# Kernel tuning notes

Hardware: AMD Instinct MI355X
Metric: run time of the kernel (lower is better)

The kernel has to match this reference:

```python
import jax, jax.numpy as jnp
import numpy as np

C = 1.0          # Poincare ball curvature
H = 8            # num_heads
EPS = 1e-15
DELTA = 1e-7
SC = np.sqrt(C)  # sqrt curvature


def _norm(x):
    return jnp.sqrt(jnp.clip(jnp.sum(x * x, -1, keepdims=True), 1e-15))


def mobius_add(x, y):
    xy = jnp.sum(x * y, -1, keepdims=True)
    x2 = jnp.sum(x * x, -1, keepdims=True)
    y2 = jnp.sum(y * y, -1, keepdims=True)
    num = (1 + 2 * C * xy + C * y2) * x + (1 - C * x2) * y
    den = 1 + 2 * C * xy + C * C * x2 * y2
    return num / (den + EPS)


def mobius_matvec(W, x):
    xn = _norm(x)
    mx = x @ W.T
    mxn = _norm(mx)
    arg = jnp.clip(SC * xn, None, 1 - 1e-5)
    return jnp.tanh(mxn / xn * jnp.arctanh(arg)) * mx / (mxn * SC)


def logmap0(x):
    xn = _norm(x)
    return jnp.arctanh(jnp.clip(SC * xn, None, 1 - 1e-5)) * x / (SC * xn)


def expmap0(u):
    un = _norm(u)
    return jnp.tanh(SC * un) * u / (SC * un)


def hyp_linear(W, b, x):
    return mobius_add(mobius_matvec(W, x), b)


def setup_inputs() -> dict:
    key = jax.random.key(0)
    ks = jax.random.split(key, 5)
    B, S, E = 2, 512, 256
    x = jax.random.normal(ks[0], (B, S, E), jnp.float32) * 0.02  # inside unit ball
    scale = float(np.sqrt(6.0 / (E + E)))  # xavier uniform bound
    Wq = jax.random.uniform(ks[1], (E, E), jnp.float32, -scale, scale)
    Wk = jax.random.uniform(ks[2], (E, E), jnp.float32, -scale, scale)
    Wv = jax.random.uniform(ks[3], (E, E), jnp.float32, -scale, scale)
    Wo = jax.random.uniform(ks[4], (E, E), jnp.float32, -scale, scale)
    z = jnp.zeros((E,), jnp.float32)
    head_scaling = jnp.ones((H, 1, 1), jnp.float32)
    return {"x": x, "Wq": Wq, "bq": z, "Wk": Wk, "bk": z, "Wv": Wv, "bv": z,
            "Wo": Wo, "bo": z, "head_scaling": head_scaling}


def reference(x, Wq, bq, Wk, bk, Wv, bv, Wo, bo, head_scaling):
    B, S, E = x.shape
    D = E // H
    q = hyp_linear(Wq, bq, x).reshape(B, S, H, D).transpose(0, 2, 1, 3)  # (B,H,S,D)
    k = hyp_linear(Wk, bk, x).reshape(B, S, H, D).transpose(0, 2, 1, 3)
    v = hyp_linear(Wv, bv, x).reshape(B, S, H, D).transpose(0, 2, 1, 3)
    max_norm = (1 - 1e-5) / SC
    q = jnp.minimum(q, max_norm)  # elementwise clamp_max, faithful to source
    k = jnp.minimum(k, max_norm)
    qn = C * jnp.sum(q * q, -1)[..., :, None]   # (B,H,Sq,1)
    kn = C * jnp.sum(k * k, -1)[..., None, :]   # (B,H,1,Sk)
    # pairwise mobius_add(-k, q): (B,H,Sq,Sk,D)
    diff = mobius_add(-k[:, :, None, :, :], q[:, :, :, None, :])
    dn = C * jnp.sum(diff * diff, -1)           # (B,H,Sq,Sk)
    denom = (1 - qn) * (1 - kn) + EPS
    a = jnp.maximum(1 + 2 * dn / denom, 1 + DELTA)
    dist = jnp.log(a + jnp.sqrt(a * a - 1))     # acosh
    scores = -dist / (head_scaling * np.sqrt(D))
    w = jax.nn.softmax(scores, -1)
    out = expmap0(jnp.einsum('bhqk,bhkd->bhqd', w, logmap0(v)))
    out = out.transpose(0, 2, 1, 3).reshape(B, S, E)
    return hyp_linear(Wo, bo, out)
```

## Files before the change

kernel.cpp:

```cpp
#include <hip/hip_runtime.h>
#include <math.h>

#define Ec 256
#define Sc 512
#define Bc 2
#define Hc 8
#define Dc 32
#define MAXNORM (1.0f - 1e-5f)
#define NEc (Bc * Sc * Ec)
#define KSQ 2
#define KSO 4
#define NROWS (Bc * Hc * Sc)

__device__ __forceinline__ float fullWaveSum(float v) {
#pragma unroll
  for (int m = 32; m >= 1; m >>= 1) v += __shfl_xor(v, m, 64);
  return v;
}
__device__ __forceinline__ float halfWaveSum(float v) {
#pragma unroll
  for (int m = 16; m >= 1; m >>= 1) v += __shfl_xor(v, m, 64);
  return v;
}
__device__ __forceinline__ float atanh_fast(float z) {
  return 0.5f * __logf((1.0f + z) / (1.0f - z));
}
__device__ __forceinline__ float tanh_fast(float a) {
  float e = __expf(-2.0f * a);
  return (1.0f - e) / (1.0f + e);
}

__global__ __launch_bounds__(128) void gemm_xwt(
    const float* __restrict__ X,
    const float* __restrict__ W0, const float* __restrict__ W1,
    const float* __restrict__ W2,
    float* __restrict__ O0, float* __restrict__ O1, float* __restrict__ O2,
    const int nk) {
  const int tid = threadIdx.x;
  const int bx = blockIdx.x;
  const int by = blockIdx.y;
  const int kz = blockIdx.z;
  const int mat = by >> 2;
  const int cb0 = (by & 3) * 64;
  const int rb0 = bx * 32;
  const int kk0 = kz * 64 * nk;
  const float* __restrict__ W = (mat == 0) ? W0 : (mat == 1) ? W1 : W2;
  float* __restrict__ O = ((mat == 0) ? O0 : (mat == 1) ? O1 : O2) + (size_t)kz * NEc;

  __shared__ float Xs[64][36];
  __shared__ float Ws[64][68];

  const int f4 = tid & 15;
  const int sub = tid >> 4;
  const int ty = tid >> 4;
  const int tx = tid & 15;

  float acc[4][4];
#pragma unroll
  for (int i = 0; i < 4; ++i)
#pragma unroll
    for (int j = 0; j < 4; ++j) acc[i][j] = 0.f;

  for (int c = 0; c < nk; ++c) {
    const int kk = kk0 + c * 64;
    __syncthreads();
#pragma unroll
    for (int i = 0; i < 4; ++i) {
      int row = sub + i * 8;
      float4 v = *(const float4*)&X[(size_t)(rb0 + row) * Ec + kk + f4 * 4];
      Xs[f4 * 4 + 0][row] = v.x;
      Xs[f4 * 4 + 1][row] = v.y;
      Xs[f4 * 4 + 2][row] = v.z;
      Xs[f4 * 4 + 3][row] = v.w;
    }
#pragma unroll
    for (int i = 0; i < 8; ++i) {
      int col = sub + i * 8;
      float4 v = *(const float4*)&W[(size_t)(cb0 + col) * Ec + kk + f4 * 4];
      Ws[f4 * 4 + 0][col] = v.x;
      Ws[f4 * 4 + 1][col] = v.y;
      Ws[f4 * 4 + 2][col] = v.z;
      Ws[f4 * 4 + 3][col] = v.w;
    }
    __syncthreads();
#pragma unroll 8
    for (int k = 0; k < 64; ++k) {
      float4 a = *(const float4*)&Xs[k][ty * 4];
      float4 b = *(const float4*)&Ws[k][tx * 4];
      float av[4] = {a.x, a.y, a.z, a.w};
      float bv[4] = {b.x, b.y, b.z, b.w};
#pragma unroll
      for (int i = 0; i < 4; ++i)
#pragma unroll
        for (int j = 0; j < 4; ++j) acc[i][j] = fmaf(av[i], bv[j], acc[i][j]);
    }
  }
#pragma unroll
  for (int i = 0; i < 4; ++i) {
    float4 o = make_float4(acc[i][0], acc[i][1], acc[i][2], acc[i][3]);
    *(float4*)&O[(size_t)(rb0 + ty * 4 + i) * Ec + cb0 + tx * 4] = o;
  }
}

__global__ __launch_bounds__(256) void qkv_stats(
    const float* __restrict__ x,
    const float* __restrict__ mxq, const float* __restrict__ mxk,
    const float* __restrict__ mxv,
    const float* __restrict__ bq, const float* __restrict__ bk,
    const float* __restrict__ bv,
    float* __restrict__ qo, float* __restrict__ ko, float* __restrict__ lvo,
    float* __restrict__ qno, float* __restrict__ kno) {
  const int t = threadIdx.x;
  const int row = blockIdx.x;
  const int b = row >> 9;
  const int s = row & (Sc - 1);
  const size_t idx = (size_t)row * Ec + t;
  const float xv = x[idx];
  float mq = 0.f, mk = 0.f, mv = 0.f;
#pragma unroll
  for (int p = 0; p < KSQ; ++p) {
    mq += mxq[idx + (size_t)p * NEc];
    mk += mxk[idx + (size_t)p * NEc];
    mv += mxv[idx + (size_t)p * NEc];
  }
  const float bb[3] = {bq[t], bk[t], bv[t]};
  const float mvals[3] = {mq, mk, mv};

  float vals[10] = {xv * xv,
                    mq * mq, mq * bb[0], bb[0] * bb[0],
                    mk * mk, mk * bb[1], bb[1] * bb[1],
                    mv * mv, mv * bb[2], bb[2] * bb[2]};
  __shared__ float red[10][4];
  __shared__ float fin[10];
#pragma unroll
  for (int i = 0; i < 10; ++i) {
    float v = fullWaveSum(vals[i]);
    if ((t & 63) == 0) red[i][t >> 6] = v;
  }
  __syncthreads();
  if (t < 10) fin[t] = red[t][0] + red[t][1] + red[t][2] + red[t][3];
  __syncthreads();

  const float x2 = fin[0];
  const float xn = sqrtf(fmaxf(x2, 1e-15f));
  const float at = atanh_fast(fminf(xn, MAXNORM));
  const int h = t >> 5;

#pragma unroll
  for (int m = 0; m < 3; ++m) {
    float mx2 = fin[1 + 3 * m];
    float mxb = fin[2 + 3 * m];
    float b2 = fin[3 + 3 * m];
    float mxn = sqrtf(fmaxf(mx2, 1e-15f));
    float scl = tanh_fast((mxn / xn) * at) / mxn;
    float mvv = scl * mvals[m];
    float X2 = scl * scl * mx2;
    float XY = scl * mxb;
    float numc = 1.0f + 2.0f * XY + b2;
    float den = 1.0f + 2.0f * XY + X2 * b2 + 1e-15f;
    float res = (numc * mvv + (1.0f - X2) * bb[m]) / den;
    if (m < 2) {
      res = fminf(res, MAXNORM);
      float s2 = halfWaveSum(res * res);
      if (m == 0) {
        qo[idx] = res;
        if ((t & 31) == 0) qno[(b * Hc + h) * Sc + s] = s2;
      } else {
        ko[idx] = res;
        if ((t & 31) == 0) kno[(b * Hc + h) * Sc + s] = s2;
      }
    } else {
      float vn2 = halfWaveSum(res * res);
      float vn = sqrtf(fmaxf(vn2, 1e-15f));
      float f = atanh_fast(fminf(vn, MAXNORM)) / vn;
      lvo[idx] = f * res;
    }
  }
}

__global__ __launch_bounds__(256) void score_kernel(
    const float* __restrict__ q, const float* __restrict__ k,
    const float* __restrict__ qn, const float* __restrict__ kn,
    const float* __restrict__ hs, float* __restrict__ P) {
  const int tid = threadIdx.x;
  const int sk0 = blockIdx.x * 64;
  const int sq0 = blockIdx.y * 64;
  const int bh = blockIdx.z;
  const int b = bh >> 3;
  const int h = bh & 7;

  __shared__ float Qs[64][32];
  __shared__ float Ks[64][32];

#pragma unroll
  for (int i = 0; i < 2; ++i) {
    int qi = tid + i * 256;
    int r = qi >> 3;
    int fd = qi & 7;
    int fsw = fd ^ ((r >> 2) & 7);
    float4 v = *(const float4*)&q[(size_t)(b * Sc + sq0 + r) * Ec + h * Dc + fd * 4];
    *(float4*)&Qs[r][fsw * 4] = v;
    float4 w = *(const float4*)&k[(size_t)(b * Sc + sk0 + r) * Ec + h * Dc + fd * 4];
    *(float4*)&Ks[r][fsw * 4] = w;
  }
  __syncthreads();

  const int ty = tid >> 4;
  const int tx = tid & 15;

  float acc[4][4];
#pragma unroll
  for (int i = 0; i < 4; ++i)
#pragma unroll
    for (int j = 0; j < 4; ++j) acc[i][j] = 0.f;

#pragma unroll
  for (int fd = 0; fd < 8; ++fd) {
    const int qsw = (fd ^ (ty & 7)) * 4;
    const int ksw = (fd ^ (tx & 7)) * 4;
    float4 a[4], bb[4];
#pragma unroll
    for (int i = 0; i < 4; ++i) a[i] = *(const float4*)&Qs[ty * 4 + i][qsw];
#pragma unroll
    for (int j = 0; j < 4; ++j) bb[j] = *(const float4*)&Ks[tx * 4 + j][ksw];
#pragma unroll
    for (int i = 0; i < 4; ++i)
#pragma unroll
      for (int j = 0; j < 4; ++j) {
        acc[i][j] = fmaf(a[i].x, bb[j].x, acc[i][j]);
        acc[i][j] = fmaf(a[i].y, bb[j].y, acc[i][j]);
        acc[i][j] = fmaf(a[i].z, bb[j].z, acc[i][j]);
        acc[i][j] = fmaf(a[i].w, bb[j].w, acc[i][j]);
      }
  }

  const float sinv = -1.0f / (hs[h] * sqrtf((float)Dc));
  float qnv[4], knv[4];
#pragma unroll
  for (int i = 0; i < 4; ++i) qnv[i] = qn[bh * Sc + sq0 + ty * 4 + i];
#pragma unroll
  for (int j = 0; j < 4; ++j) knv[j] = kn[bh * Sc + sk0 + tx * 4 + j];

#pragma unroll
  for (int i = 0; i < 4; ++i) {
    const float q2 = qnv[i];
    const float omq = 1.0f - q2;
    float4 o;
    float po[4];
#pragma unroll
    for (int j = 0; j < 4; ++j) {
      const float k2 = knv[j];
      const float kq = acc[i][j];
      const float omk = 1.0f - k2;
      float s2x2 = fmaf(-4.0f, kq, 2.0f * k2 + 2.0f * q2);
      float dden = fmaf(k2, q2, fmaf(-2.0f, kq, 1.0f)) + 1e-15f;
      float Pd = fmaf(dden, omk * omq, 1e-20f);
      float rp = __builtin_amdgcn_rcpf(Pd);
      float tt = fmaxf(s2x2 * rp, 1e-7f);
      float z = (1.0f + tt) + sqrtf(fmaf(tt, tt, tt + tt));
      po[j] = __builtin_amdgcn_exp2f(sinv * __builtin_amdgcn_logf(z));
    }
    o.x = po[0]; o.y = po[1]; o.z = po[2]; o.w = po[3];
    *(float4*)&P[((size_t)bh * Sc + sq0 + ty * 4 + i) * Sc + sk0 + tx * 4] = o;
  }
}

__global__ __launch_bounds__(256) void pv_kernel(
    const float* __restrict__ P, const float* __restrict__ lv,
    float* __restrict__ out) {
  const int tid = threadIdx.x;
  const int sq0 = blockIdx.x * 16;
  const int bh = blockIdx.y;
  const int b = bh >> 3;
  const int h = bh & 7;
  const int js = tid >> 5;
  const int rg = (tid >> 3) & 3;
  const int dq = tid & 7;

  __shared__ float Ps[16][68];
  __shared__ float lvs[64][36];
  __shared__ float accm[16][8][32];
  __shared__ float lsb[16][9];

  float4 acc[4];
#pragma unroll
  for (int i = 0; i < 4; ++i) acc[i] = make_float4(0.f, 0.f, 0.f, 0.f);
  float lsum4[4] = {0.f, 0.f, 0.f, 0.f};

#pragma unroll 1
  for (int t = 0; t < 8; ++t) {
    const int j0g = t * 64;
    {
      int pr = tid >> 4, pc = tid & 15;
      *(float4*)&Ps[pr][pc * 4] =
          *(const float4*)&P[((size_t)bh * Sc + sq0 + pr) * Sc + j0g + pc * 4];
#pragma unroll
      for (int i = 0; i < 2; ++i) {
        int qi = tid + i * 256;
        int lr = qi >> 3, lc = qi & 7;
        *(float4*)&lvs[lr][lc * 4] =
            *(const float4*)&lv[(size_t)(b * Sc + j0g + lr) * Ec + h * Dc + lc * 4];
      }
    }
    __syncthreads();

#pragma unroll
    for (int j4 = 0; j4 < 2; ++j4) {
      const int j0 = js * 8 + j4 * 4;
      float4 p[4], l[4];
#pragma unroll
      for (int i = 0; i < 4; ++i) p[i] = *(const float4*)&Ps[rg * 4 + i][j0];
#pragma unroll
      for (int c = 0; c < 4; ++c) l[c] = *(const float4*)&lvs[j0 + c][dq * 4];
#pragma unroll
      for (int i = 0; i < 4; ++i) {
        lsum4[i] += (p[i].x + p[i].y) + (p[i].z + p[i].w);
        acc[i].x = fmaf(p[i].x, l[0].x, acc[i].x);
        acc[i].y = fmaf(p[i].x, l[0].y, acc[i].y);
        acc[i].z = fmaf(p[i].x, l[0].z, acc[i].z);
        acc[i].w = fmaf(p[i].x, l[0].w, acc[i].w);
        acc[i].x = fmaf(p[i].y, l[1].x, acc[i].x);
        acc[i].y = fmaf(p[i].y, l[1].y, acc[i].y);
        acc[i].z = fmaf(p[i].y, l[1].z, acc[i].z);
        acc[i].w = fmaf(p[i].y, l[1].w, acc[i].w);
        acc[i].x = fmaf(p[i].z, l[2].x, acc[i].x);
        acc[i].y = fmaf(p[i].z, l[2].y, acc[i].y);
        acc[i].z = fmaf(p[i].z, l[2].z, acc[i].z);
        acc[i].w = fmaf(p[i].z, l[2].w, acc[i].w);
        acc[i].x = fmaf(p[i].w, l[3].x, acc[i].x);
        acc[i].y = fmaf(p[i].w, l[3].y, acc[i].y);
        acc[i].z = fmaf(p[i].w, l[3].z, acc[i].z);
        acc[i].w = fmaf(p[i].w, l[3].w, acc[i].w);
      }
    }
    __syncthreads();
  }

#pragma unroll
  for (int i = 0; i < 4; ++i)
    *(float4*)&accm[rg * 4 + i][js][dq * 4] = acc[i];
  if (dq == 0) {
#pragma unroll
    for (int i = 0; i < 4; ++i) lsb[rg * 4 + i][js] = lsum4[i];
  }
  __syncthreads();

  const int r2 = tid >> 4;
  const int dd = tid & 15;
  float o0 = 0.f, o1 = 0.f, ls = 0.f;
#pragma unroll
  for (int g = 0; g < 8; ++g) {
    float2 a2 = *(const float2*)&accm[r2][g][dd * 2];
    o0 += a2.x;
    o1 += a2.y;
    ls += lsb[r2][g];
  }
  const float li = 1.0f / ls;
  o0 *= li;
  o1 *= li;
  float un2 = fmaf(o0, o0, o1 * o1);
#pragma unroll
  for (int m = 8; m >= 1; m >>= 1) un2 += __shfl_xor(un2, m, 16);
  float un = sqrtf(fmaxf(un2, 1e-15f));
  float f = tanh_fast(un) / un;
  float2 ov = make_float2(o0 * f, o1 * f);
  *(float2*)&out[(size_t)(b * Sc + sq0 + r2) * Ec + h * Dc + dd * 2] = ov;
}

__global__ __launch_bounds__(256) void proj_stats(
    const float* __restrict__ xin, const float* __restrict__ mx,
    const float* __restrict__ bo, float* __restrict__ out) {
  const int t = threadIdx.x;
  const int row = blockIdx.x;
  const size_t idx = (size_t)row * Ec + t;
  const float xv = xin[idx];
  float m = 0.f;
#pragma unroll
  for (int p = 0; p < KSO; ++p) m += mx[idx + (size_t)p * NEc];
  const float bb = bo[t];
  float vals[4] = {xv * xv, m * m, m * bb, bb * bb};
  __shared__ float red[4][4];
  __shared__ float fin[4];
#pragma unroll
  for (int i = 0; i < 4; ++i) {
    float v = fullWaveSum(vals[i]);
    if ((t & 63) == 0) red[i][t >> 6] = v;
  }
  __syncthreads();
  if (t < 4) fin[t] = red[t][0] + red[t][1] + red[t][2] + red[t][3];
  __syncthreads();

  float x2 = fin[0], mx2 = fin[1], mxb = fin[2], b2 = fin[3];
  float xn = sqrtf(fmaxf(x2, 1e-15f));
  float mxn = sqrtf(fmaxf(mx2, 1e-15f));
  float scl = tanh_fast((mxn / xn) * atanh_fast(fminf(xn, MAXNORM))) / mxn;
  float mvv = scl * m;
  float X2 = scl * scl * mx2;
  float XY = scl * mxb;
  float numc = 1.0f + 2.0f * XY + b2;
  float den = 1.0f + 2.0f * XY + X2 * b2 + 1e-15f;
  out[idx] = (numc * mvv + (1.0f - X2) * bb) / den;
}

extern "C" void kernel_launch(void* const* d_in, const int* in_sizes, int n_in,
                              void* d_out, int out_size, void* d_ws, size_t ws_size,
                              hipStream_t stream) {
  (void)in_sizes; (void)n_in; (void)out_size; (void)ws_size;
  const float* x  = (const float*)d_in[0];
  const float* Wq = (const float*)d_in[1];
  const float* bq = (const float*)d_in[2];
  const float* Wk = (const float*)d_in[3];
  const float* bk = (const float*)d_in[4];
  const float* Wv = (const float*)d_in[5];
  const float* bv = (const float*)d_in[6];
  const float* Wo = (const float*)d_in[7];
  const float* bo = (const float*)d_in[8];
  const float* hs = (const float*)d_in[9];

  float* ws = (float*)d_ws;
  const int NE = NEc;
  const int NH = NROWS;
  float* mxq = ws;
  float* mxk = mxq + KSQ * NE;
  float* mxv = mxk + KSQ * NE;
  float* mxo = mxv + KSQ * NE;
  float* qb  = mxo + KSO * NE;
  float* kb  = qb + NE;
  float* lvb = kb + NE;
  float* aob = lvb + NE;
  float* qnb = aob + NE;
  float* knb = qnb + NH;
  float* Pb  = knb + NH;

  const int M = Bc * Sc;

  gemm_xwt<<<dim3(M / 32, 12, KSQ), 128, 0, stream>>>(x, Wq, Wk, Wv,
                                                      mxq, mxk, mxv, 2);
  qkv_stats<<<M, 256, 0, stream>>>(x, mxq, mxk, mxv, bq, bk, bv,
                                   qb, kb, lvb, qnb, knb);
  score_kernel<<<dim3(8, 8, 16), 256, 0, stream>>>(qb, kb, qnb, knb, hs, Pb);
  pv_kernel<<<dim3(32, 16), 256, 0, stream>>>(Pb, lvb, aob);
  gemm_xwt<<<dim3(M / 32, 4, KSO), 128, 0, stream>>>(aob, Wo, Wo, Wo,
                                                     mxo, mxo, mxo, 1);
  proj_stats<<<M, 256, 0, stream>>>(aob, mxo, bo, (float*)d_out);
}
```

Measured before the change: 124.7 us.

## Fuse hyperbolic score and PV kernels into single flash-style attention kernel

```diff
diff --git a/kernel.cpp b/kernel.cpp
--- a/kernel.cpp
+++ b/kernel.cpp
@@ -178,79 +178,80 @@
   }
 }
 
-__global__ __launch_bounds__(256) void score_kernel(
+__global__ __launch_bounds__(256) void attn_fused(
     const float* __restrict__ q, const float* __restrict__ k,
-    const float* __restrict__ qn, const float* __restrict__ kn,
-    const float* __restrict__ hs, float* __restrict__ P) {
+    const float* __restrict__ lv, const float* __restrict__ qn,
+    const float* __restrict__ kn, const float* __restrict__ hs,
+    float* __restrict__ out) {
   const int tid = threadIdx.x;
-  const int sk0 = blockIdx.x * 64;
-  const int sq0 = blockIdx.y * 64;
-  const int bh = blockIdx.z;
+  const int sq0 = blockIdx.x * 16;
+  const int bh = blockIdx.y;
   const int b = bh >> 3;
   const int h = bh & 7;
 
-  __shared__ float Qs[64][32];
-  __shared__ float Ks[64][32];
-
-#pragma unroll
-  for (int i = 0; i < 2; ++i) {
-    int qi = tid + i * 256;
-    int r = qi >> 3;
-    int fd = qi & 7;
-    int fsw = fd ^ ((r >> 2) & 7);
-    float4 v = *(const float4*)&q[(size_t)(b * Sc + sq0 + r) * Ec + h * Dc + fd * 4];
-    *(float4*)&Qs[r][fsw * 4] = v;
-    float4 w = *(const float4*)&k[(size_t)(b * Sc + sk0 + r) * Ec + h * Dc + fd * 4];
-    *(float4*)&Ks[r][fsw * 4] = w;
-  }
-  __syncthreads();
-
-  const int ty = tid >> 4;
-  const int tx = tid & 15;
-
-  float acc[4][4];
-#pragma unroll
-  for (int i = 0; i < 4; ++i)
-#pragma unroll
-    for (int j = 0; j < 4; ++j) acc[i][j] = 0.f;
-
-#pragma unroll
-  for (int fd = 0; fd < 8; ++fd) {
-    const int qsw = (fd ^ (ty & 7)) * 4;
-    const int ksw = (fd ^ (tx & 7)) * 4;
-    float4 a[4], bb[4];
-#pragma unroll
-    for (int i = 0; i < 4; ++i) a[i] = *(const float4*)&Qs[ty * 4 + i][qsw];
-#pragma unroll
-    for (int j = 0; j < 4; ++j) bb[j] = *(const float4*)&Ks[tx * 4 + j][ksw];
-#pragma unroll
-    for (int i = 0; i < 4; ++i)
-#pragma unroll
-      for (int j = 0; j < 4; ++j) {
-        acc[i][j] = fmaf(a[i].x, bb[j].x, acc[i][j]);
-        acc[i][j] = fmaf(a[i].y, bb[j].y, acc[i][j]);
-        acc[i][j] = fmaf(a[i].z, bb[j].z, acc[i][j]);
-        acc[i][j] = fmaf(a[i].w, bb[j].w, acc[i][j]);
-      }
-  }
-
+  __shared__ float Qst[Dc][17];
+  __shared__ float Kst[Dc][68];
+  __shared__ float LVs[2][64][36];
+  __shared__ float Pst[64][17];
+  __shared__ float knS[64];
+  __shared__ float redD[4][16];
+  __shared__ float redN[4][16];
+
+  const int r = tid & 15;
+  const int c4 = tid >> 4;
+
+  if (tid < 128) {
+    int qr = tid >> 3, dq = tid & 7;
+    float4 v = *(const float4*)&q[(size_t)(b * Sc + sq0 + qr) * Ec + h * Dc + dq * 4];
+    Qst[dq * 4 + 0][qr] = v.x;
+    Qst[dq * 4 + 1][qr] = v.y;
+    Qst[dq * 4 + 2][qr] = v.z;
+    Qst[dq * 4 + 3][qr] = v.w;
+  }
+  const float q2 = qn[bh * Sc + sq0 + r];
+  const float omq = 1.0f - q2;
   const float sinv = -1.0f / (hs[h] * sqrtf((float)Dc));
-  float qnv[4], knv[4];
-#pragma unroll
-  for (int i = 0; i < 4; ++i) qnv[i] = qn[bh * Sc + sq0 + ty * 4 + i];
-#pragma unroll
-  for (int j = 0; j < 4; ++j) knv[j] = kn[bh * Sc + sk0 + tx * 4 + j];
-
-#pragma unroll
-  for (int i = 0; i < 4; ++i) {
-    const float q2 = qnv[i];
-    const float omq = 1.0f - q2;
-    float4 o;
-    float po[4];
+
+  float out0 = 0.f, out1 = 0.f, den_acc = 0.f;
+
+  const int srow = tid >> 3;
+  const int sdq = tid & 7;
+
+  for (int t = 0; t < 8; ++t) {
+    const int j0 = t * 64;
+    const int buf = t & 1;
+#pragma unroll
+    for (int i = 0; i < 2; ++i) {
+      int row = srow + i * 32;
+      const size_t gidx = (size_t)(b * Sc + j0 + row) * Ec + h * Dc + sdq * 4;
+      float4 kv = *(const float4*)&k[gidx];
+      Kst[sdq * 4 + 0][row] = kv.x;
+      Kst[sdq * 4 + 1][row] = kv.y;
+      Kst[sdq * 4 + 2][row] = kv.z;
+      Kst[sdq * 4 + 3][row] = kv.w;
+      float4 lvv = *(const float4*)&lv[gidx];
+      *(float4*)&LVs[buf][row][sdq * 4] = lvv;
+    }
+    if (tid < 64) knS[tid] = kn[bh * Sc + j0 + tid];
+    __syncthreads();
+
+    float p[4] = {0.f, 0.f, 0.f, 0.f};
+#pragma unroll
+    for (int kk = 0; kk < Dc; ++kk) {
+      float qv = Qst[kk][r];
+      float4 kvv = *(const float4*)&Kst[kk][c4 * 4];
+      p[0] = fmaf(qv, kvv.x, p[0]);
+      p[1] = fmaf(qv, kvv.y, p[1]);
+      p[2] = fmaf(qv, kvv.z, p[2]);
+      p[3] = fmaf(qv, kvv.w, p[3]);
+    }
+    float4 k2v = *(const float4*)&knS[c4 * 4];
+    float kk2[4] = {k2v.x, k2v.y, k2v.z, k2v.w};
+    float ps = 0.f;
 #pragma unroll
     for (int j = 0; j < 4; ++j) {
-      const float k2 = knv[j];
-      const float kq = acc[i][j];
+      const float k2 = kk2[j];
+      const float kq = p[j];
       const float omk = 1.0f - k2;
       float s2x2 = fmaf(-4.0f, kq, 2.0f * k2 + 2.0f * q2);
       float dden = fmaf(k2, q2, fmaf(-2.0f, kq, 1.0f)) + 1e-15f;
@@ -258,113 +259,42 @@
       float rp = __builtin_amdgcn_rcpf(Pd);
       float tt = fmaxf(s2x2 * rp, 1e-7f);
       float z = (1.0f + tt) + sqrtf(fmaf(tt, tt, tt + tt));
-      po[j] = __builtin_amdgcn_exp2f(sinv * __builtin_amdgcn_logf(z));
-    }
-    o.x = po[0]; o.y = po[1]; o.z = po[2]; o.w = po[3];
-    *(float4*)&P[((size_t)bh * Sc + sq0 + ty * 4 + i) * Sc + sk0 + tx * 4] = o;
-  }
-}
-
-__global__ __launch_bounds__(256) void pv_kernel(
-    const float* __restrict__ P, const float* __restrict__ lv,
-    float* __restrict__ out) {
-  const int tid = threadIdx.x;
-  const int sq0 = blockIdx.x * 16;
-  const int bh = blockIdx.y;
-  const int b = bh >> 3;
-  const int h = bh & 7;
-  const int js = tid >> 5;
-  const int rg = (tid >> 3) & 3;
-  const int dq = tid & 7;
-
-  __shared__ float Ps[16][68];
-  __shared__ float lvs[64][36];
-  __shared__ float accm[16][8][32];
-  __shared__ float lsb[16][9];
-
-  float4 acc[4];
-#pragma unroll
-  for (int i = 0; i < 4; ++i) acc[i] = make_float4(0.f, 0.f, 0.f, 0.f);
-  float lsum4[4] = {0.f, 0.f, 0.f, 0.f};
-
-#pragma unroll 1
-  for (int t = 0; t < 8; ++t) {
-    const int j0g = t * 64;
-    {
-      int pr = tid >> 4, pc = tid & 15;
-      *(float4*)&Ps[pr][pc * 4] =
-          *(const float4*)&P[((size_t)bh * Sc + sq0 + pr) * Sc + j0g + pc * 4];
-#pragma unroll
-      for (int i = 0; i < 2; ++i) {
-        int qi = tid + i * 256;
-        int lr = qi >> 3, lc = qi & 7;
-        *(float4*)&lvs[lr][lc * 4] =
-            *(const float4*)&lv[(size_t)(b * Sc + j0g + lr) * Ec + h * Dc + lc * 4];
-      }
-    }
+      float po = __builtin_amdgcn_exp2f(sinv * __builtin_amdgcn_logf(z));
+      Pst[c4 * 4 + j][r] = po;
+      ps += po;
+    }
+    den_acc += ps;
     __syncthreads();
 
-#pragma unroll
-    for (int j4 = 0; j4 < 2; ++j4) {
-      const int j0 = js * 8 + j4 * 4;
-      float4 p[4], l[4];
-#pragma unroll
-      for (int i = 0; i < 4; ++i) p[i] = *(const float4*)&Ps[rg * 4 + i][j0];
-#pragma unroll
-      for (int c = 0; c < 4; ++c) l[c] = *(const float4*)&lvs[j0 + c][dq * 4];
-#pragma unroll
-      for (int i = 0; i < 4; ++i) {
-        lsum4[i] += (p[i].x + p[i].y) + (p[i].z + p[i].w);
-        acc[i].x = fmaf(p[i].x, l[0].x, acc[i].x);
-        acc[i].y = fmaf(p[i].x, l[0].y, acc[i].y);
-        acc[i].z = fmaf(p[i].x, l[0].z, acc[i].z);
-        acc[i].w = fmaf(p[i].x, l[0].w, acc[i].w);
-        acc[i].x = fmaf(p[i].y, l[1].x, acc[i].x);
-        acc[i].y = fmaf(p[i].y, l[1].y, acc[i].y);
-        acc[i].z = fmaf(p[i].y, l[1].z, acc[i].z);
-        acc[i].w = fmaf(p[i].y, l[1].w, acc[i].w);
-        acc[i].x = fmaf(p[i].z, l[2].x, acc[i].x);
-        acc[i].y = fmaf(p[i].z, l[2].y, acc[i].y);
-        acc[i].z = fmaf(p[i].z, l[2].z, acc[i].z);
-        acc[i].w = fmaf(p[i].z, l[2].w, acc[i].w);
-        acc[i].x = fmaf(p[i].w, l[3].x, acc[i].x);
-        acc[i].y = fmaf(p[i].w, l[3].y, acc[i].y);
-        acc[i].z = fmaf(p[i].w, l[3].z, acc[i].z);
-        acc[i].w = fmaf(p[i].w, l[3].w, acc[i].w);
-      }
-    }
-    __syncthreads();
-  }
-
-#pragma unroll
-  for (int i = 0; i < 4; ++i)
-    *(float4*)&accm[rg * 4 + i][js][dq * 4] = acc[i];
-  if (dq == 0) {
-#pragma unroll
-    for (int i = 0; i < 4; ++i) lsb[rg * 4 + i][js] = lsum4[i];
-  }
-  __syncthreads();
-
-  const int r2 = tid >> 4;
-  const int dd = tid & 15;
-  float o0 = 0.f, o1 = 0.f, ls = 0.f;
-#pragma unroll
-  for (int g = 0; g < 8; ++g) {
-    float2 a2 = *(const float2*)&accm[r2][g][dd * 2];
-    o0 += a2.x;
-    o1 += a2.y;
-    ls += lsb[r2][g];
-  }
-  const float li = 1.0f / ls;
-  o0 *= li;
-  o1 *= li;
+#pragma unroll 8
+    for (int j = 0; j < 64; ++j) {
+      float pj = Pst[j][r];
+      float2 l2 = *(const float2*)&LVs[buf][j][c4 * 2];
+      out0 = fmaf(pj, l2.x, out0);
+      out1 = fmaf(pj, l2.y, out1);
+    }
+  }
+
+  float d = den_acc;
+  d += __shfl_xor(d, 16, 64);
+  d += __shfl_xor(d, 32, 64);
+  const int wv = tid >> 6;
+  if ((tid & 63) < 16) redD[wv][r] = d;
+  __syncthreads();
+  const float den = redD[0][r] + redD[1][r] + redD[2][r] + redD[3][r];
+  const float li = 1.0f / den;
+  float o0 = out0 * li, o1 = out1 * li;
+
   float un2 = fmaf(o0, o0, o1 * o1);
-#pragma unroll
-  for (int m = 8; m >= 1; m >>= 1) un2 += __shfl_xor(un2, m, 16);
+  un2 += __shfl_xor(un2, 16, 64);
+  un2 += __shfl_xor(un2, 32, 64);
+  if ((tid & 63) < 16) redN[wv][r] = un2;
+  __syncthreads();
+  un2 = redN[0][r] + redN[1][r] + redN[2][r] + redN[3][r];
   float un = sqrtf(fmaxf(un2, 1e-15f));
   float f = tanh_fast(un) / un;
   float2 ov = make_float2(o0 * f, o1 * f);
-  *(float2*)&out[(size_t)(b * Sc + sq0 + r2) * Ec + h * Dc + dd * 2] = ov;
+  *(float2*)&out[(size_t)(b * Sc + sq0 + r) * Ec + h * Dc + c4 * 2] = ov;
 }
 
 __global__ __launch_bounds__(256) void proj_stats(
@@ -430,7 +360,6 @@
   float* aob = lvb + NE;
   float* qnb = aob + NE;
   float* knb = qnb + NH;
-  float* Pb  = knb + NH;
 
   const int M = Bc * Sc;
 
@@ -438,8 +367,7 @@
                                                       mxq, mxk, mxv, 2);
   qkv_stats<<<M, 256, 0, stream>>>(x, mxq, mxk, mxv, bq, bk, bv,
                                    qb, kb, lvb, qnb, knb);
-  score_kernel<<<dim3(8, 8, 16), 256, 0, stream>>>(qb, kb, qnb, knb, hs, Pb);
-  pv_kernel<<<dim3(32, 16), 256, 0, stream>>>(Pb, lvb, aob);
+  attn_fused<<<dim3(32, 16), 256, 0, stream>>>(qb, kb, lvb, qnb, knb, hs, aob);
   gemm_xwt<<<dim3(M / 32, 4, KSO), 128, 0, stream>>>(aob, Wo, Wo, Wo,
                                                      mxo, mxo, mxo, 1);
   proj_stats<<<M, 256, 0, stream>>>(aob, mxo, bo, (float*)d_out);
```

Result: slower. 133.8 us (+7.2%).

## Fuse score and PV kernels into one attention kernel without materialized P

Applied to the files above, without the earlier changes.

```diff
diff --git a/kernel.cpp b/kernel.cpp
--- a/kernel.cpp
+++ b/kernel.cpp
@@ -11,6 +11,8 @@
 #define KSQ 2
 #define KSO 4
 #define NROWS (Bc * Hc * Sc)
+#define KT 128
+#define NT (Sc / KT)
 
 __device__ __forceinline__ float fullWaveSum(float v) {
 #pragma unroll
@@ -178,140 +180,149 @@
   }
 }
 
-__global__ __launch_bounds__(256) void score_kernel(
+__global__ __launch_bounds__(256, 2) void attn_fused(
     const float* __restrict__ q, const float* __restrict__ k,
-    const float* __restrict__ qn, const float* __restrict__ kn,
-    const float* __restrict__ hs, float* __restrict__ P) {
-  const int tid = threadIdx.x;
-  const int sk0 = blockIdx.x * 64;
-  const int sq0 = blockIdx.y * 64;
-  const int bh = blockIdx.z;
-  const int b = bh >> 3;
-  const int h = bh & 7;
-
-  __shared__ float Qs[64][32];
-  __shared__ float Ks[64][32];
-
-#pragma unroll
-  for (int i = 0; i < 2; ++i) {
-    int qi = tid + i * 256;
-    int r = qi >> 3;
-    int fd = qi & 7;
-    int fsw = fd ^ ((r >> 2) & 7);
-    float4 v = *(const float4*)&q[(size_t)(b * Sc + sq0 + r) * Ec + h * Dc + fd * 4];
-    *(float4*)&Qs[r][fsw * 4] = v;
-    float4 w = *(const float4*)&k[(size_t)(b * Sc + sk0 + r) * Ec + h * Dc + fd * 4];
-    *(float4*)&Ks[r][fsw * 4] = w;
-  }
-  __syncthreads();
-
-  const int ty = tid >> 4;
-  const int tx = tid & 15;
-
-  float acc[4][4];
-#pragma unroll
-  for (int i = 0; i < 4; ++i)
-#pragma unroll
-    for (int j = 0; j < 4; ++j) acc[i][j] = 0.f;
-
-#pragma unroll
-  for (int fd = 0; fd < 8; ++fd) {
-    const int qsw = (fd ^ (ty & 7)) * 4;
-    const int ksw = (fd ^ (tx & 7)) * 4;
-    float4 a[4], bb[4];
-#pragma unroll
-    for (int i = 0; i < 4; ++i) a[i] = *(const float4*)&Qs[ty * 4 + i][qsw];
-#pragma unroll
-    for (int j = 0; j < 4; ++j) bb[j] = *(const float4*)&Ks[tx * 4 + j][ksw];
-#pragma unroll
-    for (int i = 0; i < 4; ++i)
-#pragma unroll
-      for (int j = 0; j < 4; ++j) {
-        acc[i][j] = fmaf(a[i].x, bb[j].x, acc[i][j]);
-        acc[i][j] = fmaf(a[i].y, bb[j].y, acc[i][j]);
-        acc[i][j] = fmaf(a[i].z, bb[j].z, acc[i][j]);
-        acc[i][j] = fmaf(a[i].w, bb[j].w, acc[i][j]);
-      }
-  }
-
-  const float sinv = -1.0f / (hs[h] * sqrtf((float)Dc));
-  float qnv[4], knv[4];
-#pragma unroll
-  for (int i = 0; i < 4; ++i) qnv[i] = qn[bh * Sc + sq0 + ty * 4 + i];
-#pragma unroll
-  for (int j = 0; j < 4; ++j) knv[j] = kn[bh * Sc + sk0 + tx * 4 + j];
-
-#pragma unroll
-  for (int i = 0; i < 4; ++i) {
-    const float q2 = qnv[i];
-    const float omq = 1.0f - q2;
-    float4 o;
-    float po[4];
-#pragma unroll
-    for (int j = 0; j < 4; ++j) {
-      const float k2 = knv[j];
-      const float kq = acc[i][j];
-      const float omk = 1.0f - k2;
-      float s2x2 = fmaf(-4.0f, kq, 2.0f * k2 + 2.0f * q2);
-      float dden = fmaf(k2, q2, fmaf(-2.0f, kq, 1.0f)) + 1e-15f;
-      float Pd = fmaf(dden, omk * omq, 1e-20f);
-      float rp = __builtin_amdgcn_rcpf(Pd);
-      float tt = fmaxf(s2x2 * rp, 1e-7f);
-      float z = (1.0f + tt) + sqrtf(fmaf(tt, tt, tt + tt));
-      po[j] = __builtin_amdgcn_exp2f(sinv * __builtin_amdgcn_logf(z));
-    }
-    o.x = po[0]; o.y = po[1]; o.z = po[2]; o.w = po[3];
-    *(float4*)&P[((size_t)bh * Sc + sq0 + ty * 4 + i) * Sc + sk0 + tx * 4] = o;
-  }
-}
-
-__global__ __launch_bounds__(256) void pv_kernel(
-    const float* __restrict__ P, const float* __restrict__ lv,
+    const float* __restrict__ lv, const float* __restrict__ qn,
+    const float* __restrict__ kn, const float* __restrict__ hs,
     float* __restrict__ out) {
   const int tid = threadIdx.x;
   const int sq0 = blockIdx.x * 16;
   const int bh = blockIdx.y;
   const int b = bh >> 3;
   const int h = bh & 7;
+
+  __shared__ float Qst[16][36];
+  __shared__ float Kst[32][132];
+  __shared__ float LVs[128][36];
+  __shared__ float Pst[16][132];
+  __shared__ float knS[128];
+  __shared__ float accm[16][8][32];
+  __shared__ float lsb[16][9];
+
+  const int r2 = tid >> 5;
+  const int c4 = tid & 31;
   const int js = tid >> 5;
   const int rg = (tid >> 3) & 3;
   const int dq = tid & 7;
-
-  __shared__ float Ps[16][68];
-  __shared__ float lvs[64][36];
-  __shared__ float accm[16][8][32];
-  __shared__ float lsb[16][9];
+  const int rr = tid >> 1;
+  const int half = tid & 1;
+
+  if (tid < 128) {
+    int qr = tid >> 3, dqq = tid & 7;
+    *(float4*)&Qst[qr][dqq * 4] =
+        *(const float4*)&q[(size_t)(b * Sc + sq0 + qr) * Ec + h * Dc + dqq * 4];
+  }
+  __syncthreads();
+  float4 qv0[8], qv1[8];
+#pragma unroll
+  for (int fd = 0; fd < 8; ++fd) {
+    qv0[fd] = *(const float4*)&Qst[2 * r2 + 0][fd * 4];
+    qv1[fd] = *(const float4*)&Qst[2 * r2 + 1][fd * 4];
+  }
+  const float q20 = qn[bh * Sc + sq0 + 2 * r2];
+  const float q21 = qn[bh * Sc + sq0 + 2 * r2 + 1];
+  const float omq0 = 1.0f - q20;
+  const float omq1 = 1.0f - q21;
+  const float sinv = -1.0f / (hs[h] * sqrtf((float)Dc));
 
   float4 acc[4];
 #pragma unroll
   for (int i = 0; i < 4; ++i) acc[i] = make_float4(0.f, 0.f, 0.f, 0.f);
   float lsum4[4] = {0.f, 0.f, 0.f, 0.f};
 
-#pragma unroll 1
-  for (int t = 0; t < 8; ++t) {
-    const int j0g = t * 64;
+  for (int t = 0; t < NT; ++t) {
+    const int j0g = t * KT;
+    __syncthreads();
     {
-      int pr = tid >> 4, pc = tid & 15;
-      *(float4*)&Ps[pr][pc * 4] =
-          *(const float4*)&P[((size_t)bh * Sc + sq0 + pr) * Sc + j0g + pc * 4];
-#pragma unroll
-      for (int i = 0; i < 2; ++i) {
-        int qi = tid + i * 256;
-        int lr = qi >> 3, lc = qi & 7;
-        *(float4*)&lvs[lr][lc * 4] =
-            *(const float4*)&lv[(size_t)(b * Sc + j0g + lr) * Ec + h * Dc + lc * 4];
+      const size_t gbase = (size_t)(b * Sc + j0g + rr) * Ec + h * Dc;
+#pragma unroll
+      for (int i = 0; i < 4; ++i) {
+        const int dqq = half * 4 + i;
+        float4 kv = *(const float4*)&k[gbase + dqq * 4];
+        Kst[dqq * 4 + 0][rr] = kv.x;
+        Kst[dqq * 4 + 1][rr] = kv.y;
+        Kst[dqq * 4 + 2][rr] = kv.z;
+        Kst[dqq * 4 + 3][rr] = kv.w;
+        *(float4*)&LVs[rr][dqq * 4] = *(const float4*)&lv[gbase + dqq * 4];
       }
+      if (tid < 128) knS[tid] = kn[bh * Sc + j0g + tid];
     }
     __syncthreads();
 
-#pragma unroll
-    for (int j4 = 0; j4 < 2; ++j4) {
-      const int j0 = js * 8 + j4 * 4;
+    float p0[4] = {0.f, 0.f, 0.f, 0.f};
+    float p1[4] = {0.f, 0.f, 0.f, 0.f};
+#pragma unroll
+    for (int fd = 0; fd < 8; ++fd) {
+      float4 k0 = *(const float4*)&Kst[fd * 4 + 0][c4 * 4];
+      float4 k1 = *(const float4*)&Kst[fd * 4 + 1][c4 * 4];
+      float4 k2 = *(const float4*)&Kst[fd * 4 + 2][c4 * 4];
+      float4 k3 = *(const float4*)&Kst[fd * 4 + 3][c4 * 4];
+      float4 a0 = qv0[fd];
+      float4 a1 = qv1[fd];
+      p0[0] = fmaf(a0.x, k0.x, p0[0]); p0[0] = fmaf(a0.y, k1.x, p0[0]);
+      p0[0] = fmaf(a0.z, k2.x, p0[0]); p0[0] = fmaf(a0.w, k3.x, p0[0]);
+      p0[1] = fmaf(a0.x, k0.y, p0[1]); p0[1] = fmaf(a0.y, k1.y, p0[1]);
+      p0[1] = fmaf(a0.z, k2.y, p0[1]); p0[1] = fmaf(a0.w, k3.y, p0[1]);
+      p0[2] = fmaf(a0.x, k0.z, p0[2]); p0[2] = fmaf(a0.y, k1.z, p0[2]);
+      p0[2] = fmaf(a0.z, k2.z, p0[2]); p0[2] = fmaf(a0.w, k3.z, p0[2]);
+      p0[3] = fmaf(a0.x, k0.w, p0[3]); p0[3] = fmaf(a0.y, k1.w, p0[3]);
+      p0[3] = fmaf(a0.z, k2.w, p0[3]); p0[3] = fmaf(a0.w, k3.w, p0[3]);
+      p1[0] = fmaf(a1.x, k0.x, p1[0]); p1[0] = fmaf(a1.y, k1.x, p1[0]);
+      p1[0] = fmaf(a1.z, k2.x, p1[0]); p1[0] = fmaf(a1.w, k3.x, p1[0]);
+      p1[1] = fmaf(a1.x, k0.y, p1[1]); p1[1] = fmaf(a1.y, k1.y, p1[1]);
+      p1[1] = fmaf(a1.z, k2.y, p1[1]); p1[1] = fmaf(a1.w, k3.y, p1[1]);
+      p1[2] = fmaf(a1.x, k0.z, p1[2]); p1[2] = fmaf(a1.y, k1.z, p1[2]);
+      p1[2] = fmaf(a1.z, k2.z, p1[2]); p1[2] = fmaf(a1.w, k3.z, p1[2]);
+      p1[3] = fmaf(a1.x, k0.w, p1[3]); p1[3] = fmaf(a1.y, k1.w, p1[3]);
+      p1[3] = fmaf(a1.z, k2.w, p1[3]); p1[3] = fmaf(a1.w, k3.w, p1[3]);
+    }
+
+    float4 k2v = *(const float4*)&knS[c4 * 4];
+    const float kk2[4] = {k2v.x, k2v.y, k2v.z, k2v.w};
+    {
+      float po[4];
+#pragma unroll
+      for (int j = 0; j < 4; ++j) {
+        const float k2 = kk2[j];
+        const float kq = p0[j];
+        const float omk = 1.0f - k2;
+        float s2x2 = fmaf(-4.0f, kq, 2.0f * k2 + 2.0f * q20);
+        float dden = fmaf(k2, q20, fmaf(-2.0f, kq, 1.0f)) + 1e-15f;
+        float Pd = fmaf(dden, omk * omq0, 1e-20f);
+        float rp = __builtin_amdgcn_rcpf(Pd);
+        float tt = fmaxf(s2x2 * rp, 1e-7f);
+        float z = (1.0f + tt) + sqrtf(fmaf(tt, tt, tt + tt));
+        po[j] = __builtin_amdgcn_exp2f(sinv * __builtin_amdgcn_logf(z));
+      }
+      *(float4*)&Pst[2 * r2 + 0][c4 * 4] = make_float4(po[0], po[1], po[2], po[3]);
+    }
+    {
+      float po[4];
+#pragma unroll
+      for (int j = 0; j < 4; ++j) {
+        const float k2 = kk2[j];
+        const float kq = p1[j];
+        const float omk = 1.0f - k2;
+        float s2x2 = fmaf(-4.0f, kq, 2.0f * k2 + 2.0f * q21);
+        float dden = fmaf(k2, q21, fmaf(-2.0f, kq, 1.0f)) + 1e-15f;
+        float Pd = fmaf(dden, omk * omq1, 1e-20f);
+        float rp = __builtin_amdgcn_rcpf(Pd);
+        float tt = fmaxf(s2x2 * rp, 1e-7f);
+        float z = (1.0f + tt) + sqrtf(fmaf(tt, tt, tt + tt));
+        po[j] = __builtin_amdgcn_exp2f(sinv * __builtin_amdgcn_logf(z));
+      }
+      *(float4*)&Pst[2 * r2 + 1][c4 * 4] = make_float4(po[0], po[1], po[2], po[3]);
+    }
+    __syncthreads();
+
+#pragma unroll
+    for (int j4 = 0; j4 < 4; ++j4) {
+      const int jl = js * 16 + j4 * 4;
       float4 p[4], l[4];
 #pragma unroll
-      for (int i = 0; i < 4; ++i) p[i] = *(const float4*)&Ps[rg * 4 + i][j0];
-#pragma unroll
-      for (int c = 0; c < 4; ++c) l[c] = *(const float4*)&lvs[j0 + c][dq * 4];
+      for (int i = 0; i < 4; ++i) p[i] = *(const float4*)&Pst[rg * 4 + i][jl];
+#pragma unroll
+      for (int c = 0; c < 4; ++c) l[c] = *(const float4*)&LVs[jl + c][dq * 4];
 #pragma unroll
       for (int i = 0; i < 4; ++i) {
         lsum4[i] += (p[i].x + p[i].y) + (p[i].z + p[i].w);
@@ -333,7 +344,6 @@
         acc[i].w = fmaf(p[i].w, l[3].w, acc[i].w);
       }
     }
-    __syncthreads();
   }
 
 #pragma unroll
@@ -345,15 +355,15 @@
   }
   __syncthreads();
 
-  const int r2 = tid >> 4;
+  const int r2e = tid >> 4;
   const int dd = tid & 15;
   float o0 = 0.f, o1 = 0.f, ls = 0.f;
 #pragma unroll
   for (int g = 0; g < 8; ++g) {
-    float2 a2 = *(const float2*)&accm[r2][g][dd * 2];
+    float2 a2 = *(const float2*)&accm[r2e][g][dd * 2];
     o0 += a2.x;
     o1 += a2.y;
-    ls += lsb[r2][g];
+    ls += lsb[r2e][g];
   }
   const float li = 1.0f / ls;
   o0 *= li;
@@ -364,7 +374,7 @@
   float un = sqrtf(fmaxf(un2, 1e-15f));
   float f = tanh_fast(un) / un;
   float2 ov = make_float2(o0 * f, o1 * f);
-  *(float2*)&out[(size_t)(b * Sc + sq0 + r2) * Ec + h * Dc + dd * 2] = ov;
+  *(float2*)&out[(size_t)(b * Sc + sq0 + r2e) * Ec + h * Dc + dd * 2] = ov;
 }
 
 __global__ __launch_bounds__(256) void proj_stats(
@@ -430,7 +440,6 @@
   float* aob = lvb + NE;
   float* qnb = aob + NE;
   float* knb = qnb + NH;
-  float* Pb  = knb + NH;
 
   const int M = Bc * Sc;
 
@@ -438,8 +447,7 @@
                                                       mxq, mxk, mxv, 2);
   qkv_stats<<<M, 256, 0, stream>>>(x, mxq, mxk, mxv, bq, bk, bv,
                                    qb, kb, lvb, qnb, knb);
-  score_kernel<<<dim3(8, 8, 16), 256, 0, stream>>>(qb, kb, qnb, knb, hs, Pb);
-  pv_kernel<<<dim3(32, 16), 256, 0, stream>>>(Pb, lvb, aob);
+  attn_fused<<<dim3(32, 16), 256, 0, stream>>>(qb, kb, lvb, qnb, knb, hs, aob);
   gemm_xwt<<<dim3(M / 32, 4, KSO), 128, 0, stream>>>(aob, Wo, Wo, Wo,
                                                      mxo, mxo, mxo, 1);
   proj_stats<<<M, 256, 0, stream>>>(aob, mxo, bo, (float*)d_out);
```

After: 124.6 us. Within noise of the previous version (-0.1%).
